# Kernel tuning notes

Measured on AMD Instinct MI355X. Metric: run time of the kernel, lower is better.

## Reference

```python
import jax, jax.numpy as jnp
import numpy as np
import math

B, S, H = 2, 2048, 768
NH, HD = 12, 64  # num_sparse_heads, attention_head_size
VOCAB = 30522


def setup_inputs() -> dict:
    key = jax.random.key(0)
    ks = jax.random.split(key, 6)
    scale = 0.02
    return {
        "hidden_states": jax.random.normal(ks[0], (B, S, H), dtype=jnp.float32),
        "attention_mask": jnp.zeros((B, S), dtype=jnp.float32),
        "input_ids": jax.random.randint(ks[1], (B, S), 0, VOCAB, dtype=jnp.int64) if jax.config.read('jax_enable_x64') else jax.random.randint(ks[1], (B, S), 0, VOCAB, dtype=jnp.int32),
        "ngram": 1,
        "Wq": jax.random.normal(ks[2], (H, H), dtype=jnp.float32) * scale,
        "bq": jnp.zeros((H,), dtype=jnp.float32),
        "Wk": jax.random.normal(ks[3], (H, H), dtype=jnp.float32) * scale,
        "bk": jnp.zeros((H,), dtype=jnp.float32),
    }


def reference(hidden_states, attention_mask, input_ids, ngram, Wq, bq, Wk, bk):
    # Linear projections (torch Linear: x @ W.T + b)
    q = hidden_states @ Wq.T + bq  # [B, S, H]
    k = hidden_states @ Wk.T + bk  # [B, S, H]
    # split heads -> [B, NH, S, HD]
    q = q.reshape(B, S, NH, HD).transpose(0, 2, 1, 3)
    k = k.reshape(B, S, NH, HD).transpose(0, 2, 1, 3)
    # QK^T scores, scale, additive mask over the QUERY axis (mask[:, None, :, None]), ReLU
    scores = jnp.einsum('bhqd,bhkd->bhqk', q, k) / math.sqrt(HD)
    scores = scores + attention_mask[:, None, :, None]
    probs = jax.nn.relu(scores)
    # context_layer = probs.transpose(1, 2) -> [B, S, NH, S]
    return jnp.swapaxes(probs, 1, 2)
```

## Files before the change

kernel.cpp:

```cpp
#include <hip/hip_runtime.h>
#include <hip/hip_bf16.h>
#include <stdint.h>

#define Bb  2
#define Ss  2048
#define Hh  768
#define NHh 12
#define HDd 64

typedef short bf16x8 __attribute__((ext_vector_type(8)));
typedef float f32x4  __attribute__((ext_vector_type(4)));

__device__ __forceinline__ unsigned short f2bf(float x) {
    union { float f; unsigned int u; } v; v.f = x;
    unsigned int r = v.u + 0x7fffu + ((v.u >> 16) & 1u);
    return (unsigned short)(r >> 16);
}

__global__ __launch_bounds__(256)
void proj_kernel(const float* __restrict__ hs,
                 const float* __restrict__ Wq, const float* __restrict__ bq,
                 const float* __restrict__ Wk, const float* __restrict__ bk,
                 unsigned short* __restrict__ Qb, unsigned short* __restrict__ Kb)
{
    const int zq = blockIdx.z;
    const float* __restrict__ W    = zq ? Wk : Wq;
    const float* __restrict__ bias = zq ? bk : bq;
    unsigned short* __restrict__ Out = zq ? Kb : Qb;

    const int m0 = blockIdx.x * 128;
    const int n0 = blockIdx.y * 128;

    __shared__ unsigned short As[128 * 64];
    __shared__ unsigned short Bs[128 * 64];

    const int tid  = threadIdx.x;
    const int lane = tid & 63;
    const int w    = tid >> 6;
    const int wm   = (w >> 1) * 64;
    const int wn   = (w & 1) * 64;
    const int lg   = lane >> 4;
    const int l15  = lane & 15;

    f32x4 acc[4][4] = {};

    for (int k0 = 0; k0 < 768; k0 += 64) {
        #pragma unroll
        for (int i = 0; i < 4; ++i) {
            int c   = i * 256 + tid;
            int row = c >> 3, seg = (c & 7) * 8;
            const float* ga = hs + (size_t)(m0 + row) * Hh + k0 + seg;
            const float* gb = W  + (size_t)(n0 + row) * Hh + k0 + seg;
            float4 a0 = *(const float4*)ga, a1 = *(const float4*)(ga + 4);
            float4 b0 = *(const float4*)gb, b1 = *(const float4*)(gb + 4);
            bf16x8 va, vb;
            va[0] = (short)f2bf(a0.x); va[1] = (short)f2bf(a0.y);
            va[2] = (short)f2bf(a0.z); va[3] = (short)f2bf(a0.w);
            va[4] = (short)f2bf(a1.x); va[5] = (short)f2bf(a1.y);
            va[6] = (short)f2bf(a1.z); va[7] = (short)f2bf(a1.w);
            vb[0] = (short)f2bf(b0.x); vb[1] = (short)f2bf(b0.y);
            vb[2] = (short)f2bf(b0.z); vb[3] = (short)f2bf(b0.w);
            vb[4] = (short)f2bf(b1.x); vb[5] = (short)f2bf(b1.y);
            vb[6] = (short)f2bf(b1.z); vb[7] = (short)f2bf(b1.w);
            *(bf16x8*)&As[row * 64 + seg] = va;
            *(bf16x8*)&Bs[row * 64 + seg] = vb;
        }
        __syncthreads();

        #pragma unroll
        for (int kk = 0; kk < 2; ++kk) {
            const int kof = kk * 32 + lg * 8;
            bf16x8 af[4], bfr[4];
            #pragma unroll
            for (int m = 0; m < 4; ++m)
                af[m] = *(bf16x8*)&As[(wm + m * 16 + l15) * 64 + kof];
            #pragma unroll
            for (int n = 0; n < 4; ++n)
                bfr[n] = *(bf16x8*)&Bs[(wn + n * 16 + l15) * 64 + kof];
            #pragma unroll
            for (int m = 0; m < 4; ++m)
                #pragma unroll
                for (int n = 0; n < 4; ++n)
                    acc[m][n] = __builtin_amdgcn_mfma_f32_16x16x32_bf16(
                        af[m], bfr[n], acc[m][n], 0, 0, 0);
        }
        __syncthreads();
    }

    #pragma unroll
    for (int m = 0; m < 4; ++m) {
        const int rbase = m0 + wm + m * 16 + lg * 4;
        #pragma unroll
        for (int n = 0; n < 4; ++n) {
            const int gcol = n0 + wn + n * 16 + l15;
            const float bv = bias[gcol];
            #pragma unroll
            for (int j = 0; j < 4; ++j)
                Out[(size_t)(rbase + j) * Hh + gcol] = f2bf(acc[m][n][j] + bv);
        }
    }
}

__global__ __launch_bounds__(256)
void score_kernel(const unsigned short* __restrict__ Qb,
                  const unsigned short* __restrict__ Kb,
                  const float* __restrict__ mask,
                  float* __restrict__ out)
{
    const int q0  = blockIdx.x * 128;
    const int c0  = blockIdx.y * 128;
    const int bh  = blockIdx.z;
    const int b   = bh / NHh, h = bh % NHh;

    __shared__ unsigned short Qs[128 * 64];
    __shared__ unsigned short Ks[128 * 64];

    const int tid  = threadIdx.x;
    const int lane = tid & 63;
    const int w    = tid >> 6;
    const int wm   = (w >> 1) * 64;
    const int wn   = (w & 1) * 64;
    const int lg   = lane >> 4;
    const int l15  = lane & 15;

    #pragma unroll
    for (int i = 0; i < 4; ++i) {
        int c   = i * 256 + tid;
        int row = c >> 3, seg = (c & 7) * 8;
        const uint4* gq = (const uint4*)(Qb + (size_t)(b * Ss + q0 + row) * Hh + h * HDd + seg);
        const uint4* gk = (const uint4*)(Kb + (size_t)(b * Ss + c0 + row) * Hh + h * HDd + seg);
        *(uint4*)&Qs[row * 64 + seg] = *gq;
        *(uint4*)&Ks[row * 64 + seg] = *gk;
    }
    __syncthreads();

    f32x4 acc[4][4] = {};
    #pragma unroll
    for (int kk = 0; kk < 2; ++kk) {
        const int kof = kk * 32 + lg * 8;
        bf16x8 af[4], bfr[4];
        #pragma unroll
        for (int m = 0; m < 4; ++m)
            af[m] = *(bf16x8*)&Qs[(wm + m * 16 + l15) * 64 + kof];
        #pragma unroll
        for (int n = 0; n < 4; ++n)
            bfr[n] = *(bf16x8*)&Ks[(wn + n * 16 + l15) * 64 + kof];
        #pragma unroll
        for (int m = 0; m < 4; ++m)
            #pragma unroll
            for (int n = 0; n < 4; ++n)
                acc[m][n] = __builtin_amdgcn_mfma_f32_16x16x32_bf16(
                    af[m], bfr[n], acc[m][n], 0, 0, 0);
    }

    #pragma unroll
    for (int m = 0; m < 4; ++m) {
        #pragma unroll
        for (int j = 0; j < 4; ++j) {
            const int grow = q0 + wm + m * 16 + lg * 4 + j;
            const float mv = mask[b * Ss + grow];
            #pragma unroll
            for (int n = 0; n < 4; ++n) {
                const int gcol = c0 + wn + n * 16 + l15;
                float v = acc[m][n][j] * 0.125f + mv;
                v = v > 0.f ? v : 0.f;
                out[(((size_t)b * Ss + grow) * NHh + h) * Ss + gcol] = v;
            }
        }
    }
}

extern "C" void kernel_launch(void* const* d_in, const int* in_sizes, int n_in,
                              void* d_out, int out_size, void* d_ws, size_t ws_size,
                              hipStream_t stream) {
    const float* hs   = (const float*)d_in[0];
    const float* mask = (const float*)d_in[1];
    const float* Wq = (const float*)d_in[4];
    const float* bq = (const float*)d_in[5];
    const float* Wk = (const float*)d_in[6];
    const float* bk = (const float*)d_in[7];
    float* out = (float*)d_out;

    unsigned short* Qb = (unsigned short*)d_ws;
    unsigned short* Kb = Qb + (size_t)(Bb * Ss) * Hh;

    proj_kernel<<<dim3(32, 6, 2), 256, 0, stream>>>(hs, Wq, bq, Wk, bk, Qb, Kb);

    score_kernel<<<dim3(16, 16, 24), 256, 0, stream>>>(Qb, Kb, mask, out);
}
```

Measured before the change: 123.8 us.

## Vectorize score/proj stores via transposed MFMA, pre-cast to bf16, use global_load_lds

Adds a separate cast kernel that converts hidden states and weights to bf16 once. The projection and score kernels now fill LDS with direct global-to-LDS loads instead of converting in the inner loop. Both kernels swap the MFMA operand roles so each lane's four accumulator values are contiguous in memory. That lets the epilogues use float4 (score) and 4×bf16 (projection) vector stores instead of scalar ones, targeting the store-bound output write. The cost is an extra kernel launch and an extra round trip through memory for the bf16 copies.

```diff
diff --git a/kernel.cpp b/kernel.cpp
--- a/kernel.cpp
+++ b/kernel.cpp
@@ -10,6 +10,7 @@
 
 typedef short bf16x8 __attribute__((ext_vector_type(8)));
 typedef float f32x4  __attribute__((ext_vector_type(4)));
+typedef unsigned short u16x4 __attribute__((ext_vector_type(4)));
 
 __device__ __forceinline__ unsigned short f2bf(float x) {
     union { float f; unsigned int u; } v; v.f = x;
@@ -17,14 +18,42 @@
     return (unsigned short)(r >> 16);
 }
 
+__device__ __forceinline__ void gl_lds16(const unsigned short* g, unsigned short* l) {
+    __builtin_amdgcn_global_load_lds(
+        (const __attribute__((address_space(1))) unsigned int*)g,
+        (__attribute__((address_space(3))) unsigned int*)l, 16, 0, 0);
+}
+
 __global__ __launch_bounds__(256)
-void proj_kernel(const float* __restrict__ hs,
-                 const float* __restrict__ Wq, const float* __restrict__ bq,
-                 const float* __restrict__ Wk, const float* __restrict__ bk,
+void cast_kernel(const float* __restrict__ hs, const float* __restrict__ Wq,
+                 const float* __restrict__ Wk,
+                 unsigned short* __restrict__ hsb, unsigned short* __restrict__ Wqb,
+                 unsigned short* __restrict__ Wkb)
+{
+    int cid = blockIdx.x * 256 + threadIdx.x;
+    const float* src; unsigned short* dst; int base;
+    if (cid < 393216)      { src = hs; dst = hsb; base = cid; }
+    else if (cid < 466944) { src = Wq; dst = Wqb; base = cid - 393216; }
+    else                   { src = Wk; dst = Wkb; base = cid - 466944; }
+    float4 a0 = ((const float4*)src)[(size_t)base * 2];
+    float4 a1 = ((const float4*)src)[(size_t)base * 2 + 1];
+    bf16x8 v;
+    v[0] = (short)f2bf(a0.x); v[1] = (short)f2bf(a0.y);
+    v[2] = (short)f2bf(a0.z); v[3] = (short)f2bf(a0.w);
+    v[4] = (short)f2bf(a1.x); v[5] = (short)f2bf(a1.y);
+    v[6] = (short)f2bf(a1.z); v[7] = (short)f2bf(a1.w);
+    ((bf16x8*)dst)[base] = v;
+}
+
+__global__ __launch_bounds__(256)
+void proj_kernel(const unsigned short* __restrict__ hsb,
+                 const unsigned short* __restrict__ Wqb,
+                 const unsigned short* __restrict__ Wkb,
+                 const float* __restrict__ bq, const float* __restrict__ bk,
                  unsigned short* __restrict__ Qb, unsigned short* __restrict__ Kb)
 {
     const int zq = blockIdx.z;
-    const float* __restrict__ W    = zq ? Wk : Wq;
+    const unsigned short* __restrict__ Wb = zq ? Wkb : Wqb;
     const float* __restrict__ bias = zq ? bk : bq;
     unsigned short* __restrict__ Out = zq ? Kb : Qb;
 
@@ -44,59 +73,49 @@
 
     f32x4 acc[4][4] = {};
 
-    for (int k0 = 0; k0 < 768; k0 += 64) {
+    for (int k0 = 0; k0 < Hh; k0 += 64) {
         #pragma unroll
         for (int i = 0; i < 4; ++i) {
-            int c   = i * 256 + tid;
-            int row = c >> 3, seg = (c & 7) * 8;
-            const float* ga = hs + (size_t)(m0 + row) * Hh + k0 + seg;
-            const float* gb = W  + (size_t)(n0 + row) * Hh + k0 + seg;
-            float4 a0 = *(const float4*)ga, a1 = *(const float4*)(ga + 4);
-            float4 b0 = *(const float4*)gb, b1 = *(const float4*)(gb + 4);
-            bf16x8 va, vb;
-            va[0] = (short)f2bf(a0.x); va[1] = (short)f2bf(a0.y);
-            va[2] = (short)f2bf(a0.z); va[3] = (short)f2bf(a0.w);
-            va[4] = (short)f2bf(a1.x); va[5] = (short)f2bf(a1.y);
-            va[6] = (short)f2bf(a1.z); va[7] = (short)f2bf(a1.w);
-            vb[0] = (short)f2bf(b0.x); vb[1] = (short)f2bf(b0.y);
-            vb[2] = (short)f2bf(b0.z); vb[3] = (short)f2bf(b0.w);
-            vb[4] = (short)f2bf(b1.x); vb[5] = (short)f2bf(b1.y);
-            vb[6] = (short)f2bf(b1.z); vb[7] = (short)f2bf(b1.w);
-            *(bf16x8*)&As[row * 64 + seg] = va;
-            *(bf16x8*)&Bs[row * 64 + seg] = vb;
+            int cc  = i * 256 + tid;
+            int row = cc >> 3, seg = (cc & 7) * 8;
+            gl_lds16(hsb + (size_t)(m0 + row) * Hh + k0 + seg, &As[cc * 8]);
+            gl_lds16(Wb  + (size_t)(n0 + row) * Hh + k0 + seg, &Bs[cc * 8]);
         }
         __syncthreads();
 
         #pragma unroll
         for (int kk = 0; kk < 2; ++kk) {
             const int kof = kk * 32 + lg * 8;
-            bf16x8 af[4], bfr[4];
-            #pragma unroll
-            for (int m = 0; m < 4; ++m)
-                af[m] = *(bf16x8*)&As[(wm + m * 16 + l15) * 64 + kof];
-            #pragma unroll
-            for (int n = 0; n < 4; ++n)
-                bfr[n] = *(bf16x8*)&Bs[(wn + n * 16 + l15) * 64 + kof];
-            #pragma unroll
-            for (int m = 0; m < 4; ++m)
+            bf16x8 wf[4], hf[4];
+            #pragma unroll
+            for (int i = 0; i < 4; ++i)
+                wf[i] = *(bf16x8*)&Bs[(wm + i * 16 + l15) * 64 + kof];
+            #pragma unroll
+            for (int j = 0; j < 4; ++j)
+                hf[j] = *(bf16x8*)&As[(wn + j * 16 + l15) * 64 + kof];
+            #pragma unroll
+            for (int i = 0; i < 4; ++i)
                 #pragma unroll
-                for (int n = 0; n < 4; ++n)
-                    acc[m][n] = __builtin_amdgcn_mfma_f32_16x16x32_bf16(
-                        af[m], bfr[n], acc[m][n], 0, 0, 0);
+                for (int j = 0; j < 4; ++j)
+                    acc[i][j] = __builtin_amdgcn_mfma_f32_16x16x32_bf16(
+                        wf[i], hf[j], acc[i][j], 0, 0, 0);
         }
         __syncthreads();
     }
 
     #pragma unroll
-    for (int m = 0; m < 4; ++m) {
-        const int rbase = m0 + wm + m * 16 + lg * 4;
-        #pragma unroll
-        for (int n = 0; n < 4; ++n) {
-            const int gcol = n0 + wn + n * 16 + l15;
-            const float bv = bias[gcol];
-            #pragma unroll
-            for (int j = 0; j < 4; ++j)
-                Out[(size_t)(rbase + j) * Hh + gcol] = f2bf(acc[m][n][j] + bv);
+    for (int i = 0; i < 4; ++i) {
+        const int nb = n0 + wm + i * 16 + lg * 4;
+        const float4 bv = *(const float4*)&bias[nb];
+        #pragma unroll
+        for (int j = 0; j < 4; ++j) {
+            const int m = m0 + wn + j * 16 + l15;
+            u16x4 o;
+            o[0] = f2bf(acc[i][j][0] + bv.x);
+            o[1] = f2bf(acc[i][j][1] + bv.y);
+            o[2] = f2bf(acc[i][j][2] + bv.z);
+            o[3] = f2bf(acc[i][j][3] + bv.w);
+            *(u16x4*)&Out[(size_t)m * Hh + nb] = o;
         }
     }
 }
@@ -107,10 +126,10 @@
                   const float* __restrict__ mask,
                   float* __restrict__ out)
 {
-    const int q0  = blockIdx.x * 128;
-    const int c0  = blockIdx.y * 128;
-    const int bh  = blockIdx.z;
-    const int b   = bh / NHh, h = bh % NHh;
+    const int q0 = blockIdx.x * 128;
+    const int c0 = blockIdx.y * 128;
+    const int bh = blockIdx.z;
+    const int b  = bh / NHh, h = bh % NHh;
 
     __shared__ unsigned short Qs[128 * 64];
     __shared__ unsigned short Ks[128 * 64];
@@ -125,12 +144,10 @@
 
     #pragma unroll
     for (int i = 0; i < 4; ++i) {
-        int c   = i * 256 + tid;
-        int row = c >> 3, seg = (c & 7) * 8;
-        const uint4* gq = (const uint4*)(Qb + (size_t)(b * Ss + q0 + row) * Hh + h * HDd + seg);
-        const uint4* gk = (const uint4*)(Kb + (size_t)(b * Ss + c0 + row) * Hh + h * HDd + seg);
-        *(uint4*)&Qs[row * 64 + seg] = *gq;
-        *(uint4*)&Ks[row * 64 + seg] = *gk;
+        int cc  = i * 256 + tid;
+        int row = cc >> 3, seg = (cc & 7) * 8;
+        gl_lds16(Qb + (size_t)(b * Ss + q0 + row) * Hh + h * HDd + seg, &Qs[cc * 8]);
+        gl_lds16(Kb + (size_t)(b * Ss + c0 + row) * Hh + h * HDd + seg, &Ks[cc * 8]);
     }
     __syncthreads();
 
@@ -138,34 +155,39 @@
     #pragma unroll
     for (int kk = 0; kk < 2; ++kk) {
         const int kof = kk * 32 + lg * 8;
-        bf16x8 af[4], bfr[4];
+        bf16x8 kf[4], qf[4];
         #pragma unroll
         for (int m = 0; m < 4; ++m)
-            af[m] = *(bf16x8*)&Qs[(wm + m * 16 + l15) * 64 + kof];
+            kf[m] = *(bf16x8*)&Ks[(wm + m * 16 + l15) * 64 + kof];
         #pragma unroll
         for (int n = 0; n < 4; ++n)
-            bfr[n] = *(bf16x8*)&Ks[(wn + n * 16 + l15) * 64 + kof];
+            qf[n] = *(bf16x8*)&Qs[(wn + n * 16 + l15) * 64 + kof];
         #pragma unroll
         for (int m = 0; m < 4; ++m)
             #pragma unroll
             for (int n = 0; n < 4; ++n)
                 acc[m][n] = __builtin_amdgcn_mfma_f32_16x16x32_bf16(
-                    af[m], bfr[n], acc[m][n], 0, 0, 0);
-    }
-
-    #pragma unroll
-    for (int m = 0; m < 4; ++m) {
-        #pragma unroll
-        for (int j = 0; j < 4; ++j) {
-            const int grow = q0 + wm + m * 16 + lg * 4 + j;
-            const float mv = mask[b * Ss + grow];
-            #pragma unroll
-            for (int n = 0; n < 4; ++n) {
-                const int gcol = c0 + wn + n * 16 + l15;
-                float v = acc[m][n][j] * 0.125f + mv;
-                v = v > 0.f ? v : 0.f;
-                out[(((size_t)b * Ss + grow) * NHh + h) * Ss + gcol] = v;
-            }
+                    kf[m], qf[n], acc[m][n], 0, 0, 0);
+    }
+
+    #pragma unroll
+    for (int n = 0; n < 4; ++n) {
+        const int q = q0 + wn + n * 16 + l15;
+        const float mv = mask[b * Ss + q];
+        float* orow = out + ((size_t)(b * Ss + q) * NHh + h) * Ss;
+        #pragma unroll
+        for (int m = 0; m < 4; ++m) {
+            const int kb = c0 + wm + m * 16 + lg * 4;
+            float4 o;
+            float v0 = acc[m][n][0] * 0.125f + mv;
+            float v1 = acc[m][n][1] * 0.125f + mv;
+            float v2 = acc[m][n][2] * 0.125f + mv;
+            float v3 = acc[m][n][3] * 0.125f + mv;
+            o.x = v0 > 0.f ? v0 : 0.f;
+            o.y = v1 > 0.f ? v1 : 0.f;
+            o.z = v2 > 0.f ? v2 : 0.f;
+            o.w = v3 > 0.f ? v3 : 0.f;
+            *(float4*)&orow[kb] = o;
         }
     }
 }
@@ -181,10 +203,13 @@
     const float* bk = (const float*)d_in[7];
     float* out = (float*)d_out;
 
-    unsigned short* Qb = (unsigned short*)d_ws;
-    unsigned short* Kb = Qb + (size_t)(Bb * Ss) * Hh;
-
-    proj_kernel<<<dim3(32, 6, 2), 256, 0, stream>>>(hs, Wq, bq, Wk, bk, Qb, Kb);
-
+    unsigned short* Qb  = (unsigned short*)d_ws;
+    unsigned short* Kb  = Qb  + 3145728;
+    unsigned short* hsb = Kb  + 3145728;
+    unsigned short* Wqb = hsb + 3145728;
+    unsigned short* Wkb = Wqb + 589824;
+
+    cast_kernel<<<2112, 256, 0, stream>>>(hs, Wq, Wk, hsb, Wqb, Wkb);
+    proj_kernel<<<dim3(32, 6, 2), 256, 0, stream>>>(hsb, Wqb, Wkb, bq, bk, Qb, Kb);
     score_kernel<<<dim3(16, 16, 24), 256, 0, stream>>>(Qb, Kb, mask, out);
 }
```

Result: faster. 118.0 us (-4.7%).
